# Optimization experiments

Measured on AMD Instinct MI355X. Metric: run time of the kernel, lower is better.

Reference implementation:

```python
import jax, jax.numpy as jnp
import numpy as np

T, B, I, H = 128, 128, 256, 256  # numHiddenUnits(=seq len), batch, input_size, hidden_size


def setup_inputs() -> dict:
    key = jax.random.key(0)
    ks = jax.random.split(key, 7)
    stdv = 1.0 / np.sqrt(H)
    u = lambda k, shape: jax.random.uniform(k, shape, jnp.float32, -stdv, stdv)
    return {
        "batch_x": jax.random.normal(ks[0], (T, B, I), jnp.float32),
        "initial_state": jax.random.normal(ks[1], (B, H), jnp.float32),
        "initial_state_c": jax.random.normal(ks[2], (B, H), jnp.float32),
        # distinct weights per timestep (one LSTMCell per t), stacked on dim 0
        "W_input": u(ks[3], (T, I, 4 * H)),
        "B_input": u(ks[4], (T, 4 * H)),
        "W_hidden": u(ks[5], (T, H, 4 * H)),
        "B_hidden": u(ks[6], (T, 4 * H)),
    }


def reference(batch_x, initial_state, initial_state_c, W_input, B_input, W_hidden, B_hidden):
    def step(carry, xs):
        h, c = carry
        x_t, Wi, bi, Wh, bh = xs
        gates = x_t @ Wi + bi + h @ Wh + bh  # [B, 4H]
        i_t, f_t, o_t, g_t = jnp.split(gates, 4, axis=1)  # chunk order: i, f, o, c_tilde
        c = jax.nn.sigmoid(f_t) * c + jax.nn.sigmoid(i_t) * jnp.tanh(g_t)
        h = jax.nn.sigmoid(o_t) * jnp.tanh(c)
        return (h, c), h

    (h, c), outputs = jax.lax.scan(
        step, (initial_state, initial_state_c),
        (batch_x, W_input, B_input, W_hidden, B_hidden))
    return outputs, h, c  # outputs: [T, B, H]
```

## Files before the change

### kernel.cpp

```cpp
#include <hip/hip_runtime.h>
#include <hip/hip_bf16.h>
#include <cmath>

#define T_  128
#define B_  128
#define I_  256
#define H_  256
#define G4_ 1024

using frag  = __attribute__((ext_vector_type(8))) short;
using f32x4 = __attribute__((ext_vector_type(4))) float;

__device__ __forceinline__ unsigned short bf16u(float f) {
    __hip_bfloat16 b = __float2bfloat16(f);
    return __builtin_bit_cast(unsigned short, b);
}

#define BARRIER_SEQ() do {                                   \
    __builtin_amdgcn_sched_barrier(0);                       \
    asm volatile("s_waitcnt lgkmcnt(0)" ::: "memory");       \
    __builtin_amdgcn_s_barrier();                            \
    __builtin_amdgcn_sched_barrier(0);                       \
} while (0)

__global__ __launch_bounds__(256)
void lstm_phase1(const float* __restrict__ x, const float* __restrict__ Wi,
                 const float* __restrict__ bi, const float* __restrict__ bh,
                 float* __restrict__ Gxp)
{
    __shared__ float xs[32][36];
    __shared__ float ws1[32][128];

    const int tid = threadIdx.x;
    const int bid = blockIdx.x;
    const int t  = bid >> 5;
    const int rt = (bid >> 3) & 3;
    const int cn = bid & 7;
    const int r0 = rt * 32;
    const int c0 = cn * 128;

    const int tr  = tid >> 5;
    const int tc4 = tid & 31;
    const int xrow = tid >> 3;
    const int xk0  = (tid & 7) * 4;

    float acc[4][4] = {};

    for (int kc = 0; kc < I_; kc += 32) {
        __syncthreads();
        *(float4*)&xs[xrow][xk0] =
            *(const float4*)&x[(t * B_ + r0 + xrow) * I_ + kc + xk0];
        #pragma unroll
        for (int q = 0; q < 4; ++q) {
            int s  = q * 256 + tid;
            int k  = s >> 5;
            int c4 = (s & 31) * 4;
            *(float4*)&ws1[k][c4] =
                *(const float4*)&Wi[(t * I_ + kc + k) * G4_ + c0 + c4];
        }
        __syncthreads();
        #pragma unroll
        for (int k = 0; k < 32; ++k) {
            float a0 = xs[tr * 4 + 0][k];
            float a1 = xs[tr * 4 + 1][k];
            float a2 = xs[tr * 4 + 2][k];
            float a3 = xs[tr * 4 + 3][k];
            float4 w4 = *(const float4*)&ws1[k][tc4 * 4];
            acc[0][0] += a0 * w4.x; acc[0][1] += a0 * w4.y; acc[0][2] += a0 * w4.z; acc[0][3] += a0 * w4.w;
            acc[1][0] += a1 * w4.x; acc[1][1] += a1 * w4.y; acc[1][2] += a1 * w4.z; acc[1][3] += a1 * w4.w;
            acc[2][0] += a2 * w4.x; acc[2][1] += a2 * w4.y; acc[2][2] += a2 * w4.z; acc[2][3] += a2 * w4.w;
            acc[3][0] += a3 * w4.x; acc[3][1] += a3 * w4.y; acc[3][2] += a3 * w4.z; acc[3][3] += a3 * w4.w;
        }
    }

    const int col = c0 + tc4 * 4;
    float4 b1 = *(const float4*)&bi[t * G4_ + col];
    float4 b2 = *(const float4*)&bh[t * G4_ + col];
    float bs[4] = {b1.x + b2.x, b1.y + b2.y, b1.z + b2.z, b1.w + b2.w};
    #pragma unroll
    for (int i = 0; i < 4; ++i) {
        const int gr   = r0 + tr * 4 + i;
        const int rb   = gr >> 4;
        const int rloc = gr & 15;
        #pragma unroll
        for (int j = 0; j < 4; ++j) {
            const int gc   = col + j;
            const int lane = (gc & 15) | ((rloc >> 2) << 4);
            Gxp[(((size_t)t * 8 + rb) * 64 + (gc >> 4)) * 256 + lane * 4 + (rloc & 3)]
                = acc[i][j] + bs[j];
        }
    }
}

__global__ __launch_bounds__(256)
void repack_wh(const float* __restrict__ Wh, unsigned short* __restrict__ Whp)
{
    int gid  = blockIdx.x * 256 + threadIdx.x;
    int lane = gid & 63;
    int nb   = (gid >> 6) & 63;
    int kb   = (gid >> 12) & 7;
    int t    = gid >> 15;
    int k0   = kb * 32 + (lane >> 4) * 8;
    int col  = nb * 16 + (lane & 15);
    const float* src = Wh + (size_t)(t * I_ + k0) * G4_ + col;
    unsigned short v[8];
    #pragma unroll
    for (int j = 0; j < 8; ++j) v[j] = bf16u(src[(size_t)j * G4_]);
    uint4 o;
    o.x = v[0] | ((unsigned)v[1] << 16);
    o.y = v[2] | ((unsigned)v[3] << 16);
    o.z = v[4] | ((unsigned)v[5] << 16);
    o.w = v[6] | ((unsigned)v[7] << 16);
    *(uint4*)(Whp + (size_t)gid * 8) = o;
}

__global__ __launch_bounds__(512, 1)
void lstm_rec(const float* __restrict__ h0, const float* __restrict__ c0in,
              const unsigned short* __restrict__ Whp,
              const float* __restrict__ Gxp, float* __restrict__ out,
              unsigned int* __restrict__ pub)
{
    __shared__ unsigned short h2[2][16][272];
    __shared__ float red[4][4][256];

    const int tid  = threadIdx.x;
    const int wv   = tid >> 6;
    const int lane = tid & 63;
    const int rg   = blockIdx.x & 7;
    const int sl   = blockIdx.x >> 3;
    const int r0   = rg * 16;
    const int oc0  = sl * 64;
    const int lrow = lane & 15;
    const int lhi  = lane >> 4;

    const int kh = wv >> 2;
    const int cb = wv & 3;

    {
        int row = tid >> 5;
        int cc  = (tid & 31) * 8;
        #pragma unroll
        for (int j = 0; j < 8; ++j)
            h2[0][row][cc + j] = bf16u(h0[(size_t)(r0 + row) * H_ + cc + j]);
    }

    float cst[4] = {0.f, 0.f, 0.f, 0.f};
    if (kh == 0) {
        #pragma unroll
        for (int rgi = 0; rgi < 4; ++rgi)
            cst[rgi] = c0in[(size_t)(r0 + lhi * 4 + rgi) * H_ + oc0 + cb * 16 + lrow];
    }

    int prow[12], pcol[12];
    if (kh == 1) {
        const int ltid = tid - 256;
        #pragma unroll
        for (int k = 0; k < 12; ++k) {
            int w  = ltid + k * 256;
            int rr = w / 192;
            int fc = w - rr * 192;
            prow[k] = rr;
            pcol[k] = fc + (fc >= oc0 ? 64 : 0);
        }
    }

    const unsigned short* wl = Whp + (size_t)lane * 8;
    const float*          gl = Gxp + (size_t)lane * 4;

    frag br[4][4];
    #pragma unroll
    for (int kbl = 0; kbl < 4; ++kbl)
        #pragma unroll
        for (int g = 0; g < 4; ++g)
            br[kbl][g] = *(const frag*)(wl +
                (size_t)((kh * 4 + kbl) * 64 + g * 16 + sl * 4 + cb) * 512);

    f32x4 gxr[4];
    if (kh == 0) {
        #pragma unroll
        for (int g = 0; g < 4; ++g)
            gxr[g] = *(const f32x4*)(gl +
                (size_t)((size_t)rg * 64 + g * 16 + sl * 4 + cb) * 256);
    }

    __syncthreads();

    for (int t = 0; t < T_; ++t) {
        f32x4 acc[4];
        if (kh == 0) {
            #pragma unroll
            for (int g = 0; g < 4; ++g) acc[g] = gxr[g];
            if (t + 1 < T_) {
                #pragma unroll
                for (int g = 0; g < 4; ++g)
                    gxr[g] = *(const f32x4*)(gl +
                        (size_t)(((t + 1) * 8 + rg) * 64 + g * 16 + sl * 4 + cb) * 256);
            }
        } else {
            #pragma unroll
            for (int g = 0; g < 4; ++g) acc[g] = (f32x4){0.f, 0.f, 0.f, 0.f};
        }

        #pragma unroll
        for (int kbl = 0; kbl < 4; ++kbl) {
            const int kb = kh * 4 + kbl;
            frag a = *(const frag*)&h2[t & 1][lrow][kb * 32 + lhi * 8];
            #pragma unroll
            for (int g = 0; g < 4; ++g)
                acc[g] = __builtin_amdgcn_mfma_f32_16x16x32_bf16(
                    a, br[kbl][g], acc[g], 0, 0, 0);
            if (t + 1 < T_) {
                #pragma unroll
                for (int g = 0; g < 4; ++g)
                    br[kbl][g] = *(const frag*)(wl +
                        (size_t)(((t + 1) * 8 + kb) * 64 + g * 16 + sl * 4 + cb) * 512);
            }
        }

        if (kh == 1) {
            #pragma unroll
            for (int g = 0; g < 4; ++g)
                *(f32x4*)&red[cb][g][lane * 4] = acc[g];
        }

        BARRIER_SEQ();

        if (kh == 0) {
            #pragma unroll
            for (int g = 0; g < 4; ++g)
                acc[g] += *(const f32x4*)&red[cb][g][lane * 4];
            const int colb = oc0 + cb * 16 + lrow;
            #pragma unroll
            for (int rgi = 0; rgi < 4; ++rgi) {
                const int row = lhi * 4 + rgi;
                float gi = acc[0][rgi], gf = acc[1][rgi];
                float go = acc[2][rgi], gg = acc[3][rgi];
                float i_ = __builtin_amdgcn_rcpf(1.f + __expf(-gi));
                float f_ = __builtin_amdgcn_rcpf(1.f + __expf(-gf));
                float o_ = __builtin_amdgcn_rcpf(1.f + __expf(-go));
                float gt = 1.f - 2.f * __builtin_amdgcn_rcpf(__expf(2.f * gg) + 1.f);
                float c  = f_ * cst[rgi] + i_ * gt;
                cst[rgi] = c;
                float tc = 1.f - 2.f * __builtin_amdgcn_rcpf(__expf(2.f * c) + 1.f);
                float h  = o_ * tc;
                unsigned short hb = bf16u(h);
                if (t + 1 < T_)
                    __hip_atomic_store(&pub[(size_t)(r0 + row) * H_ + colb],
                                       ((unsigned)(t + 1) << 16) | hb,
                                       __ATOMIC_RELAXED, __HIP_MEMORY_SCOPE_AGENT);
                out[(size_t)(t * B_ + r0 + row) * H_ + colb] = h;
                h2[(t + 1) & 1][row][colb] = hb;
                if (t == T_ - 1) {
                    out[(size_t)T_ * B_ * H_ + (size_t)(r0 + row) * H_ + colb] = h;
                    out[(size_t)T_ * B_ * H_ + B_ * H_ + (size_t)(r0 + row) * H_ + colb] = c;
                }
            }
        } else if (t + 1 < T_) {
            const unsigned want = (unsigned)(t + 1);
            while (true) {
                unsigned vv[12];
                #pragma unroll
                for (int k = 0; k < 12; ++k)
                    vv[k] = __hip_atomic_load(
                        &pub[(size_t)(r0 + prow[k]) * H_ + pcol[k]],
                        __ATOMIC_RELAXED, __HIP_MEMORY_SCOPE_AGENT);
                unsigned miss = 0;
                #pragma unroll
                for (int k = 0; k < 12; ++k) {
                    if ((vv[k] >> 16) == want)
                        h2[(t + 1) & 1][prow[k]][pcol[k]] =
                            (unsigned short)(vv[k] & 0xFFFFu);
                    else
                        miss = 1u;
                }
                if (!__any((int)miss)) break;
            }
        }

        BARRIER_SEQ();
    }
}

extern "C" void kernel_launch(void* const* d_in, const int* in_sizes, int n_in,
                              void* d_out, int out_size, void* d_ws, size_t ws_size,
                              hipStream_t stream) {
    const float* x  = (const float*)d_in[0];
    const float* h0 = (const float*)d_in[1];
    const float* c0 = (const float*)d_in[2];
    const float* Wi = (const float*)d_in[3];
    const float* bi = (const float*)d_in[4];
    const float* Wh = (const float*)d_in[5];
    const float* bh = (const float*)d_in[6];
    float* out = (float*)d_out;

    float*          Gxp = (float*)d_ws;
    unsigned short* Whp = (unsigned short*)((char*)d_ws + 67108864);
    unsigned int*   pub = (unsigned int*)((char*)d_ws + 134217728);

    hipMemsetAsync(pub, 0, 131072, stream);
    lstm_phase1<<<dim3(4096), dim3(256), 0, stream>>>(x, Wi, bi, bh, Gxp);
    repack_wh<<<dim3(16384), dim3(256), 0, stream>>>(Wh, Whp);
    lstm_rec<<<dim3(32), dim3(512), 0, stream>>>(h0, c0, Whp, Gxp, out, pub);
}
```

Before: 589.3 us.

## Compute input projection with bf16 MFMA and merge with Wh repack kernel

Replaces the fp32 SIMT tiled GEMM for the input-gate projection with a bf16 MFMA 16x16x32 path. Each wave loads x fragments once and converts Wi columns to bf16 on the fly, writing results straight into the packed Gxp layout. The Wh repack is folded into the same launch as extra blocks, which drops one kernel launch. The recurrent epilogue is also reordered to issue all publish atomics before the output stores, which may shorten the cross-block wait. The cost is reduced precision on the x@Wi term, and Wi is read with strided, uncached scalar loads.

```diff
diff --git a/kernel.cpp b/kernel.cpp
--- a/kernel.cpp
+++ b/kernel.cpp
@@ -10,6 +10,7 @@
 
 using frag  = __attribute__((ext_vector_type(8))) short;
 using f32x4 = __attribute__((ext_vector_type(4))) float;
+using u32x4 = __attribute__((ext_vector_type(4))) unsigned int;
 
 __device__ __forceinline__ unsigned short bf16u(float f) {
     __hip_bfloat16 b = __float2bfloat16(f);
@@ -24,94 +25,77 @@
 } while (0)
 
 __global__ __launch_bounds__(256)
-void lstm_phase1(const float* __restrict__ x, const float* __restrict__ Wi,
-                 const float* __restrict__ bi, const float* __restrict__ bh,
-                 float* __restrict__ Gxp)
+void lstm_pre(const float* __restrict__ x, const float* __restrict__ Wi,
+              const float* __restrict__ bi, const float* __restrict__ bh,
+              const float* __restrict__ Wh,
+              float* __restrict__ Gxp, unsigned short* __restrict__ Whp)
 {
-    __shared__ float xs[32][36];
-    __shared__ float ws1[32][128];
-
+    const int bid = blockIdx.x;
     const int tid = threadIdx.x;
-    const int bid = blockIdx.x;
-    const int t  = bid >> 5;
-    const int rt = (bid >> 3) & 3;
-    const int cn = bid & 7;
-    const int r0 = rt * 32;
-    const int c0 = cn * 128;
-
-    const int tr  = tid >> 5;
-    const int tc4 = tid & 31;
-    const int xrow = tid >> 3;
-    const int xk0  = (tid & 7) * 4;
-
-    float acc[4][4] = {};
-
-    for (int kc = 0; kc < I_; kc += 32) {
-        __syncthreads();
-        *(float4*)&xs[xrow][xk0] =
-            *(const float4*)&x[(t * B_ + r0 + xrow) * I_ + kc + xk0];
-        #pragma unroll
-        for (int q = 0; q < 4; ++q) {
-            int s  = q * 256 + tid;
-            int k  = s >> 5;
-            int c4 = (s & 31) * 4;
-            *(float4*)&ws1[k][c4] =
-                *(const float4*)&Wi[(t * I_ + kc + k) * G4_ + c0 + c4];
-        }
-        __syncthreads();
-        #pragma unroll
-        for (int k = 0; k < 32; ++k) {
-            float a0 = xs[tr * 4 + 0][k];
-            float a1 = xs[tr * 4 + 1][k];
-            float a2 = xs[tr * 4 + 2][k];
-            float a3 = xs[tr * 4 + 3][k];
-            float4 w4 = *(const float4*)&ws1[k][tc4 * 4];
-            acc[0][0] += a0 * w4.x; acc[0][1] += a0 * w4.y; acc[0][2] += a0 * w4.z; acc[0][3] += a0 * w4.w;
-            acc[1][0] += a1 * w4.x; acc[1][1] += a1 * w4.y; acc[1][2] += a1 * w4.z; acc[1][3] += a1 * w4.w;
-            acc[2][0] += a2 * w4.x; acc[2][1] += a2 * w4.y; acc[2][2] += a2 * w4.z; acc[2][3] += a2 * w4.w;
-            acc[3][0] += a3 * w4.x; acc[3][1] += a3 * w4.y; acc[3][2] += a3 * w4.z; acc[3][3] += a3 * w4.w;
-        }
-    }
-
-    const int col = c0 + tc4 * 4;
-    float4 b1 = *(const float4*)&bi[t * G4_ + col];
-    float4 b2 = *(const float4*)&bh[t * G4_ + col];
-    float bs[4] = {b1.x + b2.x, b1.y + b2.y, b1.z + b2.z, b1.w + b2.w};
+
+    if (bid >= 1024) {
+        int gid  = (bid - 1024) * 256 + tid;
+        int lane = gid & 63;
+        int nb   = (gid >> 6) & 63;
+        int kb   = (gid >> 12) & 7;
+        int t    = gid >> 15;
+        int k0   = kb * 32 + (lane >> 4) * 8;
+        int col  = nb * 16 + (lane & 15);
+        const float* src = Wh + (size_t)(t * I_ + k0) * G4_ + col;
+        unsigned short v[8];
+        #pragma unroll
+        for (int j = 0; j < 8; ++j) v[j] = bf16u(src[(size_t)j * G4_]);
+        uint4 o;
+        o.x = v[0] | ((unsigned)v[1] << 16);
+        o.y = v[2] | ((unsigned)v[3] << 16);
+        o.z = v[4] | ((unsigned)v[5] << 16);
+        o.w = v[6] | ((unsigned)v[7] << 16);
+        *(uint4*)(Whp + (size_t)gid * 8) = o;
+        return;
+    }
+
+    const int rb   = bid >> 7;
+    const int t    = bid & 127;
+    const int wv   = tid >> 6;
+    const int lane = tid & 63;
+    const int lrow = lane & 15;
+    const int lhi  = lane >> 4;
+
+    frag af[8];
     #pragma unroll
-    for (int i = 0; i < 4; ++i) {
-        const int gr   = r0 + tr * 4 + i;
-        const int rb   = gr >> 4;
-        const int rloc = gr & 15;
-        #pragma unroll
-        for (int j = 0; j < 4; ++j) {
-            const int gc   = col + j;
-            const int lane = (gc & 15) | ((rloc >> 2) << 4);
-            Gxp[(((size_t)t * 8 + rb) * 64 + (gc >> 4)) * 256 + lane * 4 + (rloc & 3)]
-                = acc[i][j] + bs[j];
-        }
-    }
-}
-
-__global__ __launch_bounds__(256)
-void repack_wh(const float* __restrict__ Wh, unsigned short* __restrict__ Whp)
-{
-    int gid  = blockIdx.x * 256 + threadIdx.x;
-    int lane = gid & 63;
-    int nb   = (gid >> 6) & 63;
-    int kb   = (gid >> 12) & 7;
-    int t    = gid >> 15;
-    int k0   = kb * 32 + (lane >> 4) * 8;
-    int col  = nb * 16 + (lane & 15);
-    const float* src = Wh + (size_t)(t * I_ + k0) * G4_ + col;
-    unsigned short v[8];
-    #pragma unroll
-    for (int j = 0; j < 8; ++j) v[j] = bf16u(src[(size_t)j * G4_]);
-    uint4 o;
-    o.x = v[0] | ((unsigned)v[1] << 16);
-    o.y = v[2] | ((unsigned)v[3] << 16);
-    o.z = v[4] | ((unsigned)v[5] << 16);
-    o.w = v[6] | ((unsigned)v[7] << 16);
-    *(uint4*)(Whp + (size_t)gid * 8) = o;
+    for (int kb = 0; kb < 8; ++kb) {
+        const float* ap = x + ((size_t)(t * B_ + rb * 16 + lrow) * I_ + kb * 32 + lhi * 8);
+        float4 f0 = *(const float4*)ap;
+        float4 f1 = *(const float4*)(ap + 4);
+        u32x4 p;
+        p.x = bf16u(f0.x) | ((unsigned)bf16u(f0.y) << 16);
+        p.y = bf16u(f0.z) | ((unsigned)bf16u(f0.w) << 16);
+        p.z = bf16u(f1.x) | ((unsigned)bf16u(f1.y) << 16);
+        p.w = bf16u(f1.z) | ((unsigned)bf16u(f1.w) << 16);
+        af[kb] = __builtin_bit_cast(frag, p);
+    }
+
+    for (int q = 0; q < 16; ++q) {
+        const int nb = wv * 16 + q;
+        const int gc = nb * 16 + lrow;
+        const float bias = bi[(size_t)t * G4_ + gc] + bh[(size_t)t * G4_ + gc];
+        f32x4 acc = {bias, bias, bias, bias};
+        #pragma unroll
+        for (int kb = 0; kb < 8; ++kb) {
+            const float* wp = Wi + ((size_t)(t * I_ + kb * 32 + lhi * 8) * G4_ + gc);
+            unsigned short v[8];
+            #pragma unroll
+            for (int j = 0; j < 8; ++j) v[j] = bf16u(wp[(size_t)j * G4_]);
+            u32x4 pw;
+            pw.x = v[0] | ((unsigned)v[1] << 16);
+            pw.y = v[2] | ((unsigned)v[3] << 16);
+            pw.z = v[4] | ((unsigned)v[5] << 16);
+            pw.w = v[6] | ((unsigned)v[7] << 16);
+            acc = __builtin_amdgcn_mfma_f32_16x16x32_bf16(
+                af[kb], __builtin_bit_cast(frag, pw), acc, 0, 0, 0);
+        }
+        *(f32x4*)&Gxp[(((size_t)t * 8 + rb) * 64 + nb) * 256 + lane * 4] = acc;
+    }
 }
 
 __global__ __launch_bounds__(512, 1)
@@ -230,9 +214,10 @@
             for (int g = 0; g < 4; ++g)
                 acc[g] += *(const f32x4*)&red[cb][g][lane * 4];
             const int colb = oc0 + cb * 16 + lrow;
+            float hv[4];
+            unsigned short hb[4];
             #pragma unroll
             for (int rgi = 0; rgi < 4; ++rgi) {
-                const int row = lhi * 4 + rgi;
                 float gi = acc[0][rgi], gf = acc[1][rgi];
                 float go = acc[2][rgi], gg = acc[3][rgi];
                 float i_ = __builtin_amdgcn_rcpf(1.f + __expf(-gi));
@@ -243,16 +228,28 @@
                 cst[rgi] = c;
                 float tc = 1.f - 2.f * __builtin_amdgcn_rcpf(__expf(2.f * c) + 1.f);
                 float h  = o_ * tc;
-                unsigned short hb = bf16u(h);
-                if (t + 1 < T_)
-                    __hip_atomic_store(&pub[(size_t)(r0 + row) * H_ + colb],
-                                       ((unsigned)(t + 1) << 16) | hb,
+                hv[rgi] = h;
+                hb[rgi] = bf16u(h);
+            }
+            if (t + 1 < T_) {
+                #pragma unroll
+                for (int rgi = 0; rgi < 4; ++rgi)
+                    __hip_atomic_store(&pub[(size_t)(r0 + lhi * 4 + rgi) * H_ + colb],
+                                       ((unsigned)(t + 1) << 16) | hb[rgi],
                                        __ATOMIC_RELAXED, __HIP_MEMORY_SCOPE_AGENT);
-                out[(size_t)(t * B_ + r0 + row) * H_ + colb] = h;
-                h2[(t + 1) & 1][row][colb] = hb;
-                if (t == T_ - 1) {
-                    out[(size_t)T_ * B_ * H_ + (size_t)(r0 + row) * H_ + colb] = h;
-                    out[(size_t)T_ * B_ * H_ + B_ * H_ + (size_t)(r0 + row) * H_ + colb] = c;
+            }
+            #pragma unroll
+            for (int rgi = 0; rgi < 4; ++rgi) {
+                const int row = lhi * 4 + rgi;
+                out[(size_t)(t * B_ + r0 + row) * H_ + colb] = hv[rgi];
+                h2[(t + 1) & 1][row][colb] = hb[rgi];
+            }
+            if (t == T_ - 1) {
+                #pragma unroll
+                for (int rgi = 0; rgi < 4; ++rgi) {
+                    const int row = lhi * 4 + rgi;
+                    out[(size_t)T_ * B_ * H_ + (size_t)(r0 + row) * H_ + colb] = hv[rgi];
+                    out[(size_t)T_ * B_ * H_ + B_ * H_ + (size_t)(r0 + row) * H_ + colb] = cst[rgi];
                 }
             }
         } else if (t + 1 < T_) {
@@ -298,7 +295,6 @@
     unsigned int*   pub = (unsigned int*)((char*)d_ws + 134217728);
 
     hipMemsetAsync(pub, 0, 131072, stream);
-    lstm_phase1<<<dim3(4096), dim3(256), 0, stream>>>(x, Wi, bi, bh, Gxp);
-    repack_wh<<<dim3(16384), dim3(256), 0, stream>>>(Wh, Whp);
+    lstm_pre<<<dim3(1024 + 16384), dim3(256), 0, stream>>>(x, Wi, bi, bh, Wh, Gxp, Whp);
     lstm_rec<<<dim3(32), dim3(512), 0, stream>>>(h0, c0, Whp, Gxp, out, pub);
 }
```

Measured after the change: 623.1 us. 5.8% more time.
